# Kernel tuning notes

Measured on AMD Instinct MI355X. Metric: run time of the kernel, lower is better.

The kernel has to match this reference:

```python
import jax, jax.numpy as jnp
import numpy as np
import math

B, C, D, H, W = 2, 512, 8, 16, 16
HEADS = 8
HEAD_DIM = C // HEADS
GROUPS = 8
NUM_BUCKETS = 32
MAX_DIST = 128.0
EPS = 1e-5


def setup_inputs() -> dict:
    key = jax.random.key(0)
    ks = jax.random.split(key, 4)
    return {
        "x": jax.random.normal(ks[0], (B, C, D, H, W), dtype=jnp.float32),
        "gn_w": jnp.ones((C,), jnp.float32),
        "gn_b": jnp.zeros((C,), jnp.float32),
        "qkv_w": jax.random.normal(ks[1], (3 * C, C), dtype=jnp.float32) * 0.02,
        "qkv_b": jnp.zeros((3 * C,), jnp.float32),
        "proj_w": jax.random.normal(ks[2], (C, C), dtype=jnp.float32) * 0.02,
        "proj_b": jnp.zeros((C,), jnp.float32),
        "rel_emb": jax.random.normal(ks[3], (NUM_BUCKETS,), dtype=jnp.float32) * 0.02,
    }


def _rel_pos_bias(rel_emb):
    # 3D coords flattened in (d, h, w) order, matching torch meshgrid indexing='ij'
    dd, hh, ww = jnp.meshgrid(jnp.arange(D), jnp.arange(H), jnp.arange(W), indexing='ij')
    coords = jnp.stack([dd.ravel(), hh.ravel(), ww.ravel()], axis=-1).astype(jnp.float32)  # [N,3]
    rel = coords[:, None, :] - coords[None, :, :]                      # [N,N,3]
    dist = jnp.sqrt(jnp.sum(rel * rel, axis=-1))                       # euclidean distance
    buckets = jnp.clip(jnp.floor(dist / (MAX_DIST / NUM_BUCKETS)).astype(jnp.int32), 0, NUM_BUCKETS - 1)
    return rel_emb[buckets]                                            # [N,N]


def reference(x, gn_w, gn_b, qkv_w, qkv_b, proj_w, proj_b, rel_emb):
    N = D * H * W
    # GroupNorm(8, C)
    xr = x.reshape(B, GROUPS, C // GROUPS, N)
    mu = jnp.mean(xr, axis=(2, 3), keepdims=True)
    var = jnp.var(xr, axis=(2, 3), keepdims=True)
    h = ((xr - mu) * jax.lax.rsqrt(var + EPS)).reshape(B, C, D, H, W)
    h = h * gn_w[None, :, None, None, None] + gn_b[None, :, None, None, None]
    # qkv 1x1 Conv3d == pointwise linear over channels
    qkv = jnp.einsum('bcdhw,oc->bodhw', h, qkv_w) + qkv_b[None, :, None, None, None]
    q, k, v = jnp.split(qkv, 3, axis=1)  # each [B,C,D,H,W]

    def to_heads(t):  # [B, (heads d), D,H,W] -> [B, heads, N, d]
        return t.reshape(B, HEADS, HEAD_DIM, N).transpose(0, 1, 3, 2)

    q, k, v = to_heads(q), to_heads(k), to_heads(v)
    attn = jnp.einsum('bhid,bhjd->bhij', q, k) / math.sqrt(HEAD_DIM)
    attn = attn + _rel_pos_bias(rel_emb)[None, None]
    attn = jax.nn.softmax(attn, axis=-1)
    out = jnp.einsum('bhij,bhjd->bhid', attn, v)
    out = out.transpose(0, 1, 3, 2).reshape(B, C, D, H, W)
    out = jnp.einsum('bcdhw,oc->bodhw', out, proj_w) + proj_b[None, :, None, None, None]
    return x + out
```

## Files before the change

### kernel.cpp

```cpp
#include <hip/hip_runtime.h>

typedef __attribute__((ext_vector_type(8))) __bf16 bfv8;
typedef __attribute__((ext_vector_type(4))) float f4v;
typedef __attribute__((ext_vector_type(4))) unsigned short us4v;
typedef __attribute__((ext_vector_type(8))) unsigned short us8v;

static __device__ __forceinline__ unsigned short f2bf(float f){
  union { float f; unsigned u; } v; v.f = f;
  unsigned r = v.u + 0x7fffu + ((v.u >> 16) & 1u);
  return (unsigned short)(r >> 16);
}

static __device__ __forceinline__ unsigned cvtpk(float a, float b){
  unsigned r;
  asm("v_cvt_pk_bf16_f32 %0, %1, %2" : "=v"(r) : "v"(a), "v"(b));
  return r;
}

static __device__ __forceinline__ float fexp2(float x){
#if __has_builtin(__builtin_amdgcn_exp2f)
  return __builtin_amdgcn_exp2f(x);
#else
  return __expf(x * 0.69314718056f);
#endif
}

static __device__ __forceinline__ f4v mfma16(bfv8 a, bfv8 b, f4v c){
  return __builtin_amdgcn_mfma_f32_16x16x32_bf16(a, b, c, 0, 0, 0);
}


__global__ __launch_bounds__(256) void k_prep(const float* __restrict__ qkvw,
                                              const float* __restrict__ projw,
                                              const float* __restrict__ x,
                                              unsigned short* __restrict__ WQF,
                                              unsigned short* __restrict__ WPF,
                                              float2* __restrict__ part){
  int bid = blockIdx.x;
  if (bid < 1024){
    const float* src; unsigned short* dst; int i;
    if (bid < 768){ src = qkvw; dst = WQF; i = bid*256 + threadIdx.x; }
    else          { src = projw; dst = WPF; i = (bid-768)*256 + threadIdx.x; }
    int o = i >> 7, c4 = (i & 127) << 2;
    float4 v = *(const float4*)(src + (size_t)o*512 + c4);
    us4v w; w[0]=f2bf(v.x); w[1]=f2bf(v.y); w[2]=f2bf(v.z); w[3]=f2bf(v.w);
    size_t off = (size_t)(o>>4)*8192 + ((c4>>5)<<9) + (((c4>>3)&3)<<7) + ((o&15)<<3) + (c4&7);
    *(us4v*)(dst + off) = w;
    return;
  }
  int sb = bid - 1024;
  int bg = sb >> 4, ch = sb & 15;
  const float4* base = (const float4*)(x + (size_t)bg*131072 + (size_t)ch*8192);
  float s=0.f, ss=0.f;
  #pragma unroll
  for (int it=0; it<8; ++it){
    float4 v = base[threadIdx.x + it*256];
    s  += v.x+v.y+v.z+v.w;
    ss += v.x*v.x+v.y*v.y+v.z*v.z+v.w*v.w;
  }
  #pragma unroll
  for (int off=1; off<64; off<<=1){ s += __shfl_xor(s,off); ss += __shfl_xor(ss,off); }
  __shared__ float red[8];
  int wid = threadIdx.x >> 6, l = threadIdx.x & 63;
  if (l==0){ red[wid]=s; red[wid+4]=ss; }
  __syncthreads();
  if (threadIdx.x==0)
    part[sb] = make_float2(red[0]+red[1]+red[2]+red[3],
                           red[4]+red[5]+red[6]+red[7]);
}

__global__ __launch_bounds__(256) void k_gnnorm(const float* __restrict__ x,
                                                const float2* __restrict__ part,
                                                const float* __restrict__ gnw,
                                                const float* __restrict__ gnb,
                                                unsigned short* __restrict__ AF){
  int nt = blockIdx.x & 31, ct = (blockIdx.x>>5)&7, b = blockIdx.x>>8;
  __shared__ float2 sms;
  __shared__ unsigned short tile[64][68];
  int tid = threadIdx.x;
  if (tid == 0){
    int bg = b*8 + ct;
    float s=0.f, ss=0.f;
    for (int i=0;i<16;++i){ float2 p = part[bg*16+i]; s+=p.x; ss+=p.y; }
    float mean = s * (1.f/131072.f);
    float var  = ss * (1.f/131072.f) - mean*mean;
    sms = make_float2(mean, rsqrtf(var + 1e-5f));
  }
  __syncthreads();
  float mean = sms.x, rstd = sms.y;
  int c0 = ct*64, n0 = nt*64;
  #pragma unroll
  for (int pass=0; pass<4; ++pass){
    int i = (tid>>4) + pass*16;
    int fc = tid & 15;
    int c = c0 + i;
    float w  = gnw[c]*rstd;
    float bb = gnb[c] - mean*w;
    float4 v = *(const float4*)(x + ((size_t)(b*512+c))*2048 + n0 + fc*4);
    tile[i][fc*4+0] = f2bf(v.x*w+bb);
    tile[i][fc*4+1] = f2bf(v.y*w+bb);
    tile[i][fc*4+2] = f2bf(v.z*w+bb);
    tile[i][fc*4+3] = f2bf(v.w*w+bb);
  }
  __syncthreads();
  #pragma unroll
  for (int pass=0; pass<2; ++pass){
    int r  = (tid>>3) + pass*32;
    int c8 = tid & 7;
    us8v o;
    #pragma unroll
    for (int u=0;u<8;++u) o[u] = tile[c8*8+u][r];
    int n = n0 + r, c = c0 + c8*8;
    size_t off = (size_t)(b*128 + (n>>4))*8192 + ((c>>5)<<9) + (((c>>3)&3)<<7) + ((n&15)<<3);
    *(us8v*)(AF + off) = o;
  }
}

__global__ __launch_bounds__(256) void k_qkv(const unsigned short* __restrict__ AF,
                                             const unsigned short* __restrict__ WQF,
                                             const float* __restrict__ qb,
                                             unsigned short* __restrict__ Qh,
                                             unsigned short* __restrict__ KF,
                                             unsigned short* __restrict__ VF){
  int bid = blockIdx.x;
  int ot = bid % 12; int t2 = bid / 12; int nt = t2 & 31; int b = t2 >> 5;
  int tid = threadIdx.x, wid = tid>>6, l = tid&63, lr = l&15, lg = l>>4;
  int wo = wid & 1, wn = wid >> 1;
  int n0 = nt*64 + wn*32, o0 = ot*128 + wo*64;
  f4v acc[2][4];
  #pragma unroll
  for (int a2=0;a2<2;++a2)
    #pragma unroll
    for (int s=0;s<4;++s) acc[a2][s] = (f4v){0.f,0.f,0.f,0.f};
  const unsigned short* arow = AF + (size_t)(b*128 + (n0>>4))*8192 + l*8;
  const unsigned short* brow = WQF + (size_t)(o0>>4)*8192 + l*8;
  #pragma unroll
  for (int kc=0;kc<16;++kc){
    bfv8 a0 = *(const bfv8*)(arow + kc*512);
    bfv8 a1 = *(const bfv8*)(arow + 8192 + kc*512);
    #pragma unroll
    for (int s=0;s<4;++s){
      bfv8 bb = *(const bfv8*)(brow + s*8192 + kc*512);
      acc[0][s] = mfma16(a0, bb, acc[0][s]);
      acc[1][s] = mfma16(a1, bb, acc[1][s]);
    }
  }
  #pragma unroll
  for (int s=0;s<4;++s){
    int o = o0 + s*16 + lr;
    float bias = qb[o];
    int seg = o >> 9, oo = o & 511, h = oo>>6, dd = oo&63;
    size_t hb = (size_t)(b*8+h)*131072;
    #pragma unroll
    for (int a2=0;a2<2;++a2){
      #pragma unroll
      for (int r=0;r<4;++r){
        int n = n0 + a2*16 + lg*4 + r;
        unsigned short val = f2bf(acc[a2][s][r] + bias);
        if (seg==0)
          Qh[hb + (size_t)n*64 + dd] = val;
        else if (seg==1)
          KF[hb + (n>>4)*1024 + (dd>>5)*512 + ((dd>>3)&3)*128 + (n&15)*8 + (dd&7)] = val;
        else
          VF[hb + (n>>5)*2048 + (dd>>4)*512 + ((n>>3)&3)*128 + (dd&15)*8 + (n&7)] = val;
      }
    }
  }
}

__global__ __launch_bounds__(256, 4) void k_attn(const unsigned short* __restrict__ Qh,
                                                 const unsigned short* __restrict__ KF,
                                                 const unsigned short* __restrict__ VF,
                                                 const float* __restrict__ rel,
                                                 unsigned short* __restrict__ AOF){
  int did = blockIdx.x;
  int bh = (did & 7)*2 + ((did >> 9) & 1);
  int qt = (did >> 3) & 63;
  int tid = threadIdx.x, wid = tid>>6, l = tid&63, lr = l&15, lg = l>>4;
  __shared__ float slut[32];
  __shared__ __align__(16) char smem[16384];
  if (tid < 32){
    int bkt = (tid>=1)+(tid>=4)+(tid>=9)+(tid>=16)+(tid>=25);
    slut[tid] = rel[bkt] * 1.44269504f;
  }
  __syncthreads();
  int q0 = qt*32;
  int dq = q0 >> 8, hqA = (q0 >> 4) & 15, hqB = hqA + 1;
  int swsq[4];
  #pragma unroll
  for (int r=0;r<4;++r){ int sw = lr - (lg*4+r); swsq[r] = sw*sw; }
  const unsigned short* Qb = Qh + (size_t)bh*131072;
  const unsigned short* Kb = KF + (size_t)bh*131072;
  const unsigned short* Vb = VF + (size_t)bh*131072;
  bfv8 qf0A = *(const bfv8*)(Qb + (size_t)(q0+lr)*64 + lg*8);
  bfv8 qf1A = *(const bfv8*)(Qb + (size_t)(q0+lr)*64 + 32 + lg*8);
  bfv8 qf0B = *(const bfv8*)(Qb + (size_t)(q0+16+lr)*64 + lg*8);
  bfv8 qf1B = *(const bfv8*)(Qb + (size_t)(q0+16+lr)*64 + 32 + lg*8);
  f4v oA[4], oB[4];
  #pragma unroll
  for (int i2=0;i2<4;++i2){ oA[i2] = (f4v){0.f,0.f,0.f,0.f}; oB[i2] = (f4v){0.f,0.f,0.f,0.f}; }
  float lsA = 0.f, lsB = 0.f;
  char* pwA = smem + wid*4096;
  char* pwB = pwA + 2048;
  int swz = (lr&7)<<4;
  for (int it=0; it<8; ++it){
    int itg = wid*8 + it;
    f4v sa[4], sb[4];
    #pragma unroll
    for (int t=0;t<4;++t){ sa[t] = (f4v){0.f,0.f,0.f,0.f}; sb[t] = (f4v){0.f,0.f,0.f,0.f}; }
    #pragma unroll
    for (int t=0;t<4;++t){
      const unsigned short* kb = Kb + (size_t)(itg*4 + t)*1024 + l*8;
      bfv8 k0 = *(const bfv8*)kb;
      bfv8 k1 = *(const bfv8*)(kb + 512);
      sa[t] = mfma16(k0, qf0A, sa[t]);
      sa[t] = mfma16(k1, qf1A, sa[t]);
      sb[t] = mfma16(k0, qf0B, sb[t]);
      sb[t] = mfma16(k1, qf1B, sb[t]);
    }
    int dj = itg>>2; int sd = dq-dj; int sds = sd*sd;
    int hj0 = (itg&3)*4;
    #pragma unroll
    for (int t=0;t<4;++t){
      int sh = hqA - (hj0+t); int sdh = sds + sh*sh;
      float p0 = fexp2(fmaf(sa[t][0], 0.180336878f, slut[(sdh+swsq[0])>>4]));
      float p1 = fexp2(fmaf(sa[t][1], 0.180336878f, slut[(sdh+swsq[1])>>4]));
      float p2 = fexp2(fmaf(sa[t][2], 0.180336878f, slut[(sdh+swsq[2])>>4]));
      float p3 = fexp2(fmaf(sa[t][3], 0.180336878f, slut[(sdh+swsq[3])>>4]));
      lsA += (p0+p1)+(p2+p3);
      uint2 w; w.x = cvtpk(p0,p1); w.y = cvtpk(p2,p3);
      *(uint2*)(pwA + lr*128 + ((32*t + 8*lg) ^ swz)) = w;
    }
    #pragma unroll
    for (int t=0;t<4;++t){
      int sh = hqB - (hj0+t); int sdh = sds + sh*sh;
      float p0 = fexp2(fmaf(sb[t][0], 0.180336878f, slut[(sdh+swsq[0])>>4]));
      float p1 = fexp2(fmaf(sb[t][1], 0.180336878f, slut[(sdh+swsq[1])>>4]));
      float p2 = fexp2(fmaf(sb[t][2], 0.180336878f, slut[(sdh+swsq[2])>>4]));
      float p3 = fexp2(fmaf(sb[t][3], 0.180336878f, slut[(sdh+swsq[3])>>4]));
      lsB += (p0+p1)+(p2+p3);
      uint2 w; w.x = cvtpk(p0,p1); w.y = cvtpk(p2,p3);
      *(uint2*)(pwB + lr*128 + ((32*t + 8*lg) ^ swz)) = w;
    }
    #pragma unroll
    for (int kt=0;kt<2;++kt){
      bfv8 pfA = *(const bfv8*)(pwA + lr*128 + ((64*kt + 16*lg) ^ swz));
      bfv8 pfB = *(const bfv8*)(pwB + lr*128 + ((64*kt + 16*lg) ^ swz));
      const unsigned short* vb = Vb + (size_t)(itg*2 + kt)*2048 + l*8;
      #pragma unroll
      for (int d2=0;d2<4;++d2){
        bfv8 vf = *(const bfv8*)(vb + d2*512);
        oA[d2] = mfma16(pfA, vf, oA[d2]);
        oB[d2] = mfma16(pfB, vf, oB[d2]);
      }
    }
  }
  lsA += __shfl_xor(lsA, 16); lsA += __shfl_xor(lsA, 32);
  lsB += __shfl_xor(lsB, 16); lsB += __shfl_xor(lsB, 32);
  __syncthreads();
  float* sOf = (float*)smem;
  float* sls = (float*)(smem + 32*68*4);
  #pragma unroll 1
  for (int p=0; p<4; ++p){
    if (wid == p){
      if (p == 0){
        #pragma unroll
        for (int r=0;r<4;++r){
          #pragma unroll
          for (int d2=0;d2<4;++d2){
            sOf[(lg*4+r)*68 + d2*16+lr] = oA[d2][r];
            sOf[(16+lg*4+r)*68 + d2*16+lr] = oB[d2][r];
          }
        }
        if (l < 16){ sls[l] = lsA; sls[16+l] = lsB; }
      } else {
        #pragma unroll
        for (int r=0;r<4;++r){
          #pragma unroll
          for (int d2=0;d2<4;++d2){
            sOf[(lg*4+r)*68 + d2*16+lr] += oA[d2][r];
            sOf[(16+lg*4+r)*68 + d2*16+lr] += oB[d2][r];
          }
        }
        if (l < 16){ sls[l] += lsA; sls[16+l] += lsB; }
      }
    }
    __syncthreads();
  }
  int b = bh>>3, h = bh&7;
  int col = tid & 63, rw = tid >> 6;
  #pragma unroll
  for (int k=0;k<8;++k){
    int row = rw*8 + k;
    float v = sOf[row*68 + col] / sls[row];
    int n = q0 + row;
    size_t off = (size_t)(b*128 + (n>>4))*8192 + (size_t)(h*2 + (col>>5))*512
               + ((col>>3)&3)*128 + (n&15)*8 + (col&7);
    AOF[off] = f2bf(v);
  }
}

__global__ __launch_bounds__(256) void k_proj(const unsigned short* __restrict__ AOF,
                                              const unsigned short* __restrict__ WPF,
                                              const float* __restrict__ pb,
                                              const float* __restrict__ x,
                                              float* __restrict__ out){
  int nt = blockIdx.x & 31, ot = (blockIdx.x>>5)&7, b = blockIdx.x>>8;
  int tid = threadIdx.x, wid = tid>>6, l = tid&63, lr = l&15, lg = l>>4;
  int o0 = ot*64 + wid*16, n0 = nt*64;
  f4v acc[4];
  #pragma unroll
  for (int t=0;t<4;++t) acc[t] = (f4v){0.f,0.f,0.f,0.f};
  const unsigned short* arow = WPF + (size_t)(o0>>4)*8192 + l*8;
  const unsigned short* brow = AOF + (size_t)(b*128 + (n0>>4))*8192 + l*8;
  #pragma unroll
  for (int kc=0;kc<16;++kc){
    bfv8 a = *(const bfv8*)(arow + kc*512);
    #pragma unroll
    for (int t=0;t<4;++t){
      bfv8 bb = *(const bfv8*)(brow + t*8192 + kc*512);
      acc[t] = mfma16(a, bb, acc[t]);
    }
  }
  #pragma unroll
  for (int r=0;r<4;++r){
    int o = o0 + lg*4 + r;
    float bias = pb[o];
    #pragma unroll
    for (int t=0;t<4;++t){
      int n = n0 + t*16 + lr;
      size_t idx = ((size_t)(b*512)+o)*2048 + n;
      out[idx] = acc[t][r] + bias + x[idx];
    }
  }
}

extern "C" void kernel_launch(void* const* d_in, const int* in_sizes, int n_in,
                              void* d_out, int out_size, void* d_ws, size_t ws_size,
                              hipStream_t stream){
  const float* x     = (const float*)d_in[0];
  const float* gnw   = (const float*)d_in[1];
  const float* gnb   = (const float*)d_in[2];
  const float* qkvw  = (const float*)d_in[3];
  const float* qkvb  = (const float*)d_in[4];
  const float* projw = (const float*)d_in[5];
  const float* projb = (const float*)d_in[6];
  const float* rel   = (const float*)d_in[7];
  float* out = (float*)d_out;
  char* ws = (char*)d_ws;
  float2* part           = (float2*)ws;
  unsigned short* WQF    = (unsigned short*)(ws + 4096);
  unsigned short* WPF    = (unsigned short*)(ws + 1576960);
  unsigned short* AF     = (unsigned short*)(ws + 2101248);
  unsigned short* Qh     = (unsigned short*)(ws + 6295552);
  unsigned short* KF     = (unsigned short*)(ws + 10489856);
  unsigned short* VF     = (unsigned short*)(ws + 14684160);
  unsigned short* AOF    = (unsigned short*)(ws + 18878464);

  hipLaunchKernelGGL(k_prep,   dim3(1280), dim3(256), 0, stream, qkvw, projw, x, WQF, WPF, part);
  hipLaunchKernelGGL(k_gnnorm, dim3(512),  dim3(256), 0, stream, x, part, gnw, gnb, AF);
  hipLaunchKernelGGL(k_qkv,    dim3(768),  dim3(256), 0, stream, AF, WQF, qkvb, Qh, KF, VF);
  hipLaunchKernelGGL(k_attn,   dim3(1024), dim3(256), 0, stream, Qh, KF, VF, rel, AOF);
  hipLaunchKernelGGL(k_proj,   dim3(512),  dim3(256), 0, stream, AOF, WPF, projb, x, out);
}
```

Before: 70.53 us.

## Stream K tiles via async global-to-LDS double buffering in attention loop

Replaces the direct global loads of K fragments with global_load_lds into a per-wave double-buffered LDS staging area, prefetching the next K tile while the current one is processed. The loop is restructured to process one 16-key tile per iteration (fully unrolled over 32 tiles), interleaving score, exp and PV MFMA steps at finer granularity. It adds 16KB of LDS, which may reduce occupancy, and relies on manual vmcnt waits that must match the compiler's outstanding load counts (V loads are also global), which risks both over-waiting and correctness.

After: 75.80 us. 7.5% more time.

```diff
diff --git a/kernel.cpp b/kernel.cpp
--- a/kernel.cpp
+++ b/kernel.cpp
@@ -27,6 +27,12 @@
 
 static __device__ __forceinline__ f4v mfma16(bfv8 a, bfv8 b, f4v c){
   return __builtin_amdgcn_mfma_f32_16x16x32_bf16(a, b, c, 0, 0, 0);
+}
+
+static __device__ __forceinline__ void gload16(const void* g, void* l){
+  __builtin_amdgcn_global_load_lds((const __attribute__((address_space(1))) unsigned int*)g,
+                                   (__attribute__((address_space(3))) unsigned int*)l,
+                                   16, 0, 0);
 }
 
 
@@ -178,6 +184,7 @@
   int qt = (did >> 3) & 63;
   int tid = threadIdx.x, wid = tid>>6, l = tid&63, lr = l&15, lg = l>>4;
   __shared__ float slut[32];
+  __shared__ __align__(16) char ksmem[16384];
   __shared__ __align__(16) char smem[16384];
   if (tid < 32){
     int bkt = (tid>=1)+(tid>=4)+(tid>=9)+(tid>=16)+(tid>=25);
@@ -202,51 +209,61 @@
   float lsA = 0.f, lsB = 0.f;
   char* pwA = smem + wid*4096;
   char* pwB = pwA + 2048;
+  char* kst = ksmem + wid*4096;
   int swz = (lr&7)<<4;
-  for (int it=0; it<8; ++it){
-    int itg = wid*8 + it;
-    f4v sa[4], sb[4];
-    #pragma unroll
-    for (int t=0;t<4;++t){ sa[t] = (f4v){0.f,0.f,0.f,0.f}; sb[t] = (f4v){0.f,0.f,0.f,0.f}; }
-    #pragma unroll
-    for (int t=0;t<4;++t){
-      const unsigned short* kb = Kb + (size_t)(itg*4 + t)*1024 + l*8;
-      bfv8 k0 = *(const bfv8*)kb;
-      bfv8 k1 = *(const bfv8*)(kb + 512);
-      sa[t] = mfma16(k0, qf0A, sa[t]);
-      sa[t] = mfma16(k1, qf1A, sa[t]);
-      sb[t] = mfma16(k0, qf0B, sb[t]);
-      sb[t] = mfma16(k1, qf1B, sb[t]);
-    }
-    int dj = itg>>2; int sd = dq-dj; int sds = sd*sd;
-    int hj0 = (itg&3)*4;
-    #pragma unroll
-    for (int t=0;t<4;++t){
-      int sh = hqA - (hj0+t); int sdh = sds + sh*sh;
-      float p0 = fexp2(fmaf(sa[t][0], 0.180336878f, slut[(sdh+swsq[0])>>4]));
-      float p1 = fexp2(fmaf(sa[t][1], 0.180336878f, slut[(sdh+swsq[1])>>4]));
-      float p2 = fexp2(fmaf(sa[t][2], 0.180336878f, slut[(sdh+swsq[2])>>4]));
-      float p3 = fexp2(fmaf(sa[t][3], 0.180336878f, slut[(sdh+swsq[3])>>4]));
+  int tg0 = wid*32;
+  {
+    const unsigned short* src = Kb + (size_t)tg0*1024 + l*8;
+    gload16(src,        kst);
+    gload16(src + 512,  kst + 1024);
+  }
+  #pragma unroll
+  for (int tt=0; tt<32; ++tt){
+    int tg = tg0 + tt;
+    char* kb_cur = kst + (tt&1)*2048;
+    if (tt < 31){
+      const unsigned short* src = Kb + (size_t)(tg+1)*1024 + l*8;
+      char* kb_nxt = kst + ((tt+1)&1)*2048;
+      gload16(src,       kb_nxt);
+      gload16(src + 512, kb_nxt + 1024);
+      asm volatile("s_waitcnt vmcnt(2)" ::: "memory");
+    } else {
+      asm volatile("s_waitcnt vmcnt(0)" ::: "memory");
+    }
+    bfv8 k0 = *(const bfv8*)(kb_cur + l*16);
+    bfv8 k1 = *(const bfv8*)(kb_cur + 1024 + l*16);
+    f4v sa = (f4v){0.f,0.f,0.f,0.f}, sb = (f4v){0.f,0.f,0.f,0.f};
+    sa = mfma16(k0, qf0A, sa);
+    sa = mfma16(k1, qf1A, sa);
+    sb = mfma16(k0, qf0B, sb);
+    sb = mfma16(k1, qf1B, sb);
+    int dj = tg>>4; int sd = dq-dj; int sds = sd*sd;
+    int hj = tg & 15;
+    {
+      int sh = hqA - hj; int sdh = sds + sh*sh;
+      float p0 = fexp2(fmaf(sa[0], 0.180336878f, slut[(sdh+swsq[0])>>4]));
+      float p1 = fexp2(fmaf(sa[1], 0.180336878f, slut[(sdh+swsq[1])>>4]));
+      float p2 = fexp2(fmaf(sa[2], 0.180336878f, slut[(sdh+swsq[2])>>4]));
+      float p3 = fexp2(fmaf(sa[3], 0.180336878f, slut[(sdh+swsq[3])>>4]));
       lsA += (p0+p1)+(p2+p3);
       uint2 w; w.x = cvtpk(p0,p1); w.y = cvtpk(p2,p3);
-      *(uint2*)(pwA + lr*128 + ((32*t + 8*lg) ^ swz)) = w;
-    }
-    #pragma unroll
-    for (int t=0;t<4;++t){
-      int sh = hqB - (hj0+t); int sdh = sds + sh*sh;
-      float p0 = fexp2(fmaf(sb[t][0], 0.180336878f, slut[(sdh+swsq[0])>>4]));
-      float p1 = fexp2(fmaf(sb[t][1], 0.180336878f, slut[(sdh+swsq[1])>>4]));
-      float p2 = fexp2(fmaf(sb[t][2], 0.180336878f, slut[(sdh+swsq[2])>>4]));
-      float p3 = fexp2(fmaf(sb[t][3], 0.180336878f, slut[(sdh+swsq[3])>>4]));
+      *(uint2*)(pwA + lr*128 + ((32*(tt&3) + 8*lg) ^ swz)) = w;
+    }
+    {
+      int sh = hqB - hj; int sdh = sds + sh*sh;
+      float p0 = fexp2(fmaf(sb[0], 0.180336878f, slut[(sdh+swsq[0])>>4]));
+      float p1 = fexp2(fmaf(sb[1], 0.180336878f, slut[(sdh+swsq[1])>>4]));
+      float p2 = fexp2(fmaf(sb[2], 0.180336878f, slut[(sdh+swsq[2])>>4]));
+      float p3 = fexp2(fmaf(sb[3], 0.180336878f, slut[(sdh+swsq[3])>>4]));
       lsB += (p0+p1)+(p2+p3);
       uint2 w; w.x = cvtpk(p0,p1); w.y = cvtpk(p2,p3);
-      *(uint2*)(pwB + lr*128 + ((32*t + 8*lg) ^ swz)) = w;
-    }
-    #pragma unroll
-    for (int kt=0;kt<2;++kt){
-      bfv8 pfA = *(const bfv8*)(pwA + lr*128 + ((64*kt + 16*lg) ^ swz));
-      bfv8 pfB = *(const bfv8*)(pwB + lr*128 + ((64*kt + 16*lg) ^ swz));
-      const unsigned short* vb = Vb + (size_t)(itg*2 + kt)*2048 + l*8;
+      *(uint2*)(pwB + lr*128 + ((32*(tt&3) + 8*lg) ^ swz)) = w;
+    }
+    if (tt & 1){
+      int kth = (tt>>1) & 1;
+      bfv8 pfA = *(const bfv8*)(pwA + lr*128 + ((64*kth + 16*lg) ^ swz));
+      bfv8 pfB = *(const bfv8*)(pwB + lr*128 + ((64*kth + 16*lg) ^ swz));
+      const unsigned short* vb = Vb + (size_t)(tg>>1)*2048 + l*8;
       #pragma unroll
       for (int d2=0;d2<4;++d2){
         bfv8 vf = *(const bfv8*)(vb + d2*512);
```

## Stage K/V tiles in LDS with double-buffered async loads shared across waves

Applied to the files above, without the earlier changes.

The attention kernel now gives each wave its own 32 queries over the full key range, instead of splitting keys across waves and reducing partial outputs. K/V tiles are loaded once per block into double-buffered LDS with global_load_lds and shared by four waves, which cuts redundant global reads and removes the cross-wave reduction through shared memory. The grid shrinks from 1024 to 256 blocks and the occupancy hint is dropped. This risks low parallelism on a large-CU GPU and adds barrier stalls every iteration.

New measurement: 89.76 us. 1.27x slower.

```diff
diff --git a/kernel.cpp b/kernel.cpp
--- a/kernel.cpp
+++ b/kernel.cpp
@@ -27,6 +27,12 @@
 
 static __device__ __forceinline__ f4v mfma16(bfv8 a, bfv8 b, f4v c){
   return __builtin_amdgcn_mfma_f32_16x16x32_bf16(a, b, c, 0, 0, 0);
+}
+
+static __device__ __forceinline__ void gload16(const void* g, void* l){
+  __builtin_amdgcn_global_load_lds((const __attribute__((address_space(1))) unsigned int*)g,
+                                   (__attribute__((address_space(3))) unsigned int*)l,
+                                   16, 0, 0);
 }
 
 
@@ -168,30 +174,30 @@
   }
 }
 
-__global__ __launch_bounds__(256, 4) void k_attn(const unsigned short* __restrict__ Qh,
-                                                 const unsigned short* __restrict__ KF,
-                                                 const unsigned short* __restrict__ VF,
-                                                 const float* __restrict__ rel,
-                                                 unsigned short* __restrict__ AOF){
+__global__ __launch_bounds__(256) void k_attn(const unsigned short* __restrict__ Qh,
+                                              const unsigned short* __restrict__ KF,
+                                              const unsigned short* __restrict__ VF,
+                                              const float* __restrict__ rel,
+                                              unsigned short* __restrict__ AOF){
   int did = blockIdx.x;
-  int bh = (did & 7)*2 + ((did >> 9) & 1);
-  int qt = (did >> 3) & 63;
+  int bh = (did & 7)*2 + ((did >> 7) & 1);
+  int qt = (did >> 3) & 15;
   int tid = threadIdx.x, wid = tid>>6, l = tid&63, lr = l&15, lg = l>>4;
   __shared__ float slut[32];
-  __shared__ __align__(16) char smem[16384];
+  __shared__ __align__(16) char kvs[2][16384];
+  __shared__ __align__(16) char pbufs[4][4096];
   if (tid < 32){
     int bkt = (tid>=1)+(tid>=4)+(tid>=9)+(tid>=16)+(tid>=25);
     slut[tid] = rel[bkt] * 1.44269504f;
   }
-  __syncthreads();
-  int q0 = qt*32;
+  int q0 = qt*128 + wid*32;
   int dq = q0 >> 8, hqA = (q0 >> 4) & 15, hqB = hqA + 1;
   int swsq[4];
   #pragma unroll
   for (int r=0;r<4;++r){ int sw = lr - (lg*4+r); swsq[r] = sw*sw; }
   const unsigned short* Qb = Qh + (size_t)bh*131072;
-  const unsigned short* Kb = KF + (size_t)bh*131072;
-  const unsigned short* Vb = VF + (size_t)bh*131072;
+  const char* Kb = (const char*)(KF + (size_t)bh*131072);
+  const char* Vb = (const char*)(VF + (size_t)bh*131072);
   bfv8 qf0A = *(const bfv8*)(Qb + (size_t)(q0+lr)*64 + lg*8);
   bfv8 qf1A = *(const bfv8*)(Qb + (size_t)(q0+lr)*64 + 32 + lg*8);
   bfv8 qf0B = *(const bfv8*)(Qb + (size_t)(q0+16+lr)*64 + lg*8);
@@ -200,26 +206,50 @@
   #pragma unroll
   for (int i2=0;i2<4;++i2){ oA[i2] = (f4v){0.f,0.f,0.f,0.f}; oB[i2] = (f4v){0.f,0.f,0.f,0.f}; }
   float lsA = 0.f, lsB = 0.f;
-  char* pwA = smem + wid*4096;
+  char* pwA = pbufs[wid];
   char* pwB = pwA + 2048;
   int swz = (lr&7)<<4;
-  for (int it=0; it<8; ++it){
-    int itg = wid*8 + it;
+  int wb16 = wid*1024 + (l&63)*16;
+  {
+    char* dst = kvs[0] + wid*1024;
+    const char* ks = Kb + wb16;
+    const char* vs = Vb + wb16;
+    gload16(ks,        dst);
+    gload16(ks + 4096, dst + 4096);
+    gload16(vs,        dst + 8192);
+    gload16(vs + 4096, dst + 12288);
+  }
+  __syncthreads();
+  #pragma unroll 2
+  for (int i=0; i<32; ++i){
+    char* kv = kvs[i&1];
+    if (i < 31){
+      char* dst = kvs[(i+1)&1] + wid*1024;
+      const char* ks = Kb + (size_t)(i+1)*8192 + wb16;
+      const char* vs = Vb + (size_t)(i+1)*8192 + wb16;
+      gload16(ks,        dst);
+      gload16(ks + 4096, dst + 4096);
+      gload16(vs,        dst + 8192);
+      gload16(vs + 4096, dst + 12288);
+      asm volatile("s_waitcnt vmcnt(4)" ::: "memory");
+    } else {
+      asm volatile("s_waitcnt vmcnt(0)" ::: "memory");
+    }
+    __builtin_amdgcn_s_barrier();
     f4v sa[4], sb[4];
     #pragma unroll
     for (int t=0;t<4;++t){ sa[t] = (f4v){0.f,0.f,0.f,0.f}; sb[t] = (f4v){0.f,0.f,0.f,0.f}; }
     #pragma unroll
     for (int t=0;t<4;++t){
-      const unsigned short* kb = Kb + (size_t)(itg*4 + t)*1024 + l*8;
-      bfv8 k0 = *(const bfv8*)kb;
-      bfv8 k1 = *(const bfv8*)(kb + 512);
+      bfv8 k0 = *(const bfv8*)(kv + t*2048 + l*16);
+      bfv8 k1 = *(const bfv8*)(kv + t*2048 + 1024 + l*16);
       sa[t] = mfma16(k0, qf0A, sa[t]);
       sa[t] = mfma16(k1, qf1A, sa[t]);
       sb[t] = mfma16(k0, qf0B, sb[t]);
       sb[t] = mfma16(k1, qf1B, sb[t]);
     }
-    int dj = itg>>2; int sd = dq-dj; int sds = sd*sd;
-    int hj0 = (itg&3)*4;
+    int dj = i>>2; int sd = dq-dj; int sds = sd*sd;
+    int hj0 = (i&3)*4;
     #pragma unroll
     for (int t=0;t<4;++t){
       int sh = hqA - (hj0+t); int sdh = sds + sh*sh;
@@ -246,57 +276,32 @@
     for (int kt=0;kt<2;++kt){
       bfv8 pfA = *(const bfv8*)(pwA + lr*128 + ((64*kt + 16*lg) ^ swz));
       bfv8 pfB = *(const bfv8*)(pwB + lr*128 + ((64*kt + 16*lg) ^ swz));
-      const unsigned short* vb = Vb + (size_t)(itg*2 + kt)*2048 + l*8;
+      const char* vt = kv + 8192 + kt*4096;
       #pragma unroll
       for (int d2=0;d2<4;++d2){
-        bfv8 vf = *(const bfv8*)(vb + d2*512);
+        bfv8 vf = *(const bfv8*)(vt + d2*1024 + l*16);
         oA[d2] = mfma16(pfA, vf, oA[d2]);
         oB[d2] = mfma16(pfB, vf, oB[d2]);
       }
     }
+    __builtin_amdgcn_s_barrier();
   }
   lsA += __shfl_xor(lsA, 16); lsA += __shfl_xor(lsA, 32);
   lsB += __shfl_xor(lsB, 16); lsB += __shfl_xor(lsB, 32);
-  __syncthreads();
-  float* sOf = (float*)smem;
-  float* sls = (float*)(smem + 32*68*4);
-  #pragma unroll 1
-  for (int p=0; p<4; ++p){
-    if (wid == p){
-      if (p == 0){
-        #pragma unroll
-        for (int r=0;r<4;++r){
-          #pragma unroll
-          for (int d2=0;d2<4;++d2){
-            sOf[(lg*4+r)*68 + d2*16+lr] = oA[d2][r];
-            sOf[(16+lg*4+r)*68 + d2*16+lr] = oB[d2][r];
-          }
-        }
-        if (l < 16){ sls[l] = lsA; sls[16+l] = lsB; }
-      } else {
-        #pragma unroll
-        for (int r=0;r<4;++r){
-          #pragma unroll
-          for (int d2=0;d2<4;++d2){
-            sOf[(lg*4+r)*68 + d2*16+lr] += oA[d2][r];
-            sOf[(16+lg*4+r)*68 + d2*16+lr] += oB[d2][r];
-          }
-        }
-        if (l < 16){ sls[l] += lsA; sls[16+l] += lsB; }
-      }
-    }
-    __syncthreads();
-  }
   int b = bh>>3, h = bh&7;
-  int col = tid & 63, rw = tid >> 6;
-  #pragma unroll
-  for (int k=0;k<8;++k){
-    int row = rw*8 + k;
-    float v = sOf[row*68 + col] / sls[row];
-    int n = q0 + row;
-    size_t off = (size_t)(b*128 + (n>>4))*8192 + (size_t)(h*2 + (col>>5))*512
-               + ((col>>3)&3)*128 + (n&15)*8 + (col&7);
-    AOF[off] = f2bf(v);
+  #pragma unroll
+  for (int r=0;r<4;++r){
+    float invA = 1.f / __shfl(lsA, lg*4+r);
+    float invB = 1.f / __shfl(lsB, lg*4+r);
+    #pragma unroll
+    for (int d2=0;d2<4;++d2){
+      int c = h*64 + d2*16 + lr;
+      size_t cpart = ((size_t)(c>>5)<<9) + (((c>>3)&3)<<7) + (c&7);
+      int nA = q0 + lg*4 + r;
+      int nB = nA + 16;
+      AOF[(size_t)(b*128 + (nA>>4))*8192 + cpart + (nA&15)*8] = f2bf(oA[d2][r]*invA);
+      AOF[(size_t)(b*128 + (nB>>4))*8192 + cpart + (nB&15)*8] = f2bf(oB[d2][r]*invB);
+    }
   }
 }
 
@@ -360,6 +365,6 @@
   hipLaunchKernelGGL(k_prep,   dim3(1280), dim3(256), 0, stream, qkvw, projw, x, WQF, WPF, part);
   hipLaunchKernelGGL(k_gnnorm, dim3(512),  dim3(256), 0, stream, x, part, gnw, gnb, AF);
   hipLaunchKernelGGL(k_qkv,    dim3(768),  dim3(256), 0, stream, AF, WQF, qkvb, Qh, KF, VF);
-  hipLaunchKernelGGL(k_attn,   dim3(1024), dim3(256), 0, stream, Qh, KF, VF, rel, AOF);
+  hipLaunchKernelGGL(k_attn,   dim3(256),  dim3(256), 0, stream, Qh, KF, VF, rel, AOF);
   hipLaunchKernelGGL(k_proj,   dim3(512),  dim3(256), 0, stream, AOF, WPF, projb, x, out);
 }
```
